# Optimization experiments

Measured on AMD Instinct MI355X. Metric: run time of the kernel, lower is better.

## Reference

```python
import jax, jax.numpy as jnp
import numpy as np


def setup_inputs() -> dict:
    key = jax.random.key(0)
    kx, kt = jax.random.split(key)
    b, n, d = 4, 4096, 1024
    x = jax.random.normal(kx, (b, n, d), dtype=jnp.float32)
    t = jax.random.normal(kt, (n, d), dtype=jnp.float32)
    return {"x": x, "t": t}


def reference(x, t):
    # y[b,i,d] = sum_{j<=i} t[i-j,d] * x[b,j,d]
    # Causal depthwise Toeplitz matvec == linear convolution truncated to n.
    # Computed via FFT along the sequence axis (zero-pad to 2n so the
    # circular convolution equals the linear one on the first n outputs).
    b, n, d = x.shape
    L = 2 * n
    xf = jnp.fft.rfft(x.astype(jnp.float32), n=L, axis=1)        # (b, L/2+1, d) complex
    tf = jnp.fft.rfft(t.astype(jnp.float32), n=L, axis=0)        # (L/2+1, d) complex
    y = jnp.fft.irfft(xf * tf[None], n=L, axis=1)[:, :n, :]      # (b, n, d)
    return y.astype(x.dtype)
```

## Files before the change

kernel.cpp:

```cpp
#include <hip/hip_runtime.h>

#define NT 512
#define SCL (1.0f / 8192.0f)
#define PI_F 3.14159265358979323846f

__device__ __forceinline__ int P(int i) { return i ^ ((i >> 5) & 31); }

__device__ __forceinline__ float2 cmul(float2 a, float2 b) {
  return make_float2(a.x * b.x - a.y * b.y, a.x * b.y + a.y * b.x);
}
__device__ __forceinline__ float2 csqr(float2 a) {
  return make_float2(a.x * a.x - a.y * a.y, 2.f * a.x * a.y);
}
__device__ __forceinline__ float2 cadd(float2 a, float2 b) { return make_float2(a.x + b.x, a.y + b.y); }
__device__ __forceinline__ float2 csub(float2 a, float2 b) { return make_float2(a.x - b.x, a.y - b.y); }
__device__ __forceinline__ float2 cmuli (float2 a) { return make_float2(-a.y,  a.x); }
__device__ __forceinline__ float2 cmulmi(float2 a) { return make_float2( a.y, -a.x); }

constexpr float RT2 = 0.70710678118654752440f;
constexpr float CQ1 = 0.92387953251128675613f;
constexpr float SQ1 = 0.38268343236508977173f;
constexpr float C8x[4] = {1.f,  RT2, 0.f, -RT2};
constexpr float C8y[4] = {0.f, -RT2, -1.f, -RT2};
constexpr float C16x[8] = {1.f,  CQ1,  RT2,  SQ1, 0.f, -SQ1, -RT2, -CQ1};
constexpr float C16y[8] = {0.f, -SQ1, -RT2, -CQ1, -1.f, -CQ1, -RT2, -SQ1};

template<bool UNIT>
__device__ __forceinline__ void r8_fwd(float2* e, float2 b) {
  float2 b2, b4;
  if (!UNIT) { b2 = csqr(b); b4 = csqr(b2); }
  #pragma unroll
  for (int j = 0; j < 4; ++j) {
    float2 u = e[j], v = e[j + 4];
    float2 d = csub(u, v);
    e[j] = cadd(u, v);
    float2 c8 = make_float2(C8x[j], C8y[j]);
    if (UNIT) e[j + 4] = (j == 0) ? d : cmul(d, c8);
    else      e[j + 4] = cmul(d, (j == 0) ? b : cmul(b, c8));
  }
  #pragma unroll
  for (int o = 0; o < 8; o += 4) {
    #pragma unroll
    for (int j = 0; j < 2; ++j) {
      float2 u = e[o + j], v = e[o + j + 2];
      float2 d = csub(u, v);
      e[o + j] = cadd(u, v);
      if (UNIT) e[o + j + 2] = (j == 0) ? d : cmulmi(d);
      else      e[o + j + 2] = cmul(d, (j == 0) ? b2 : cmulmi(b2));
    }
  }
  #pragma unroll
  for (int o = 0; o < 8; o += 2) {
    float2 u = e[o], v = e[o + 1];
    float2 d = csub(u, v);
    e[o] = cadd(u, v);
    e[o + 1] = UNIT ? d : cmul(d, b4);
  }
}

template<bool UNIT>
__device__ __forceinline__ void r8_inv(float2* e, float2 g) {
  float2 g2, g4;
  if (!UNIT) { g2 = csqr(g); g4 = csqr(g2); }
  #pragma unroll
  for (int o = 0; o < 8; o += 2) {
    float2 t = UNIT ? e[o + 1] : cmul(e[o + 1], g4);
    float2 u = e[o];
    e[o] = cadd(u, t); e[o + 1] = csub(u, t);
  }
  #pragma unroll
  for (int o = 0; o < 8; o += 4) {
    #pragma unroll
    for (int j = 0; j < 2; ++j) {
      float2 v = e[o + j + 2];
      float2 t;
      if (UNIT) t = (j == 0) ? v : cmuli(v);
      else      t = cmul(v, (j == 0) ? g2 : cmuli(g2));
      float2 u = e[o + j];
      e[o + j] = cadd(u, t); e[o + j + 2] = csub(u, t);
    }
  }
  #pragma unroll
  for (int j = 0; j < 4; ++j) {
    float2 v = e[j + 4];
    float2 t;
    float2 c8c = make_float2(C8x[j], -C8y[j]);
    if (UNIT) t = (j == 0) ? v : cmul(v, c8c);
    else      t = cmul(v, (j == 0) ? g : cmul(g, c8c));
    float2 u = e[j];
    e[j] = cadd(u, t); e[j + 4] = csub(u, t);
  }
}

__device__ __forceinline__ void d8f(float4* cb, int base, int G, float2 b) {
  float2 lo[8], hi[8];
  #pragma unroll
  for (int j = 0; j < 8; ++j) {
    float4 q = cb[P(base + G * j)];
    lo[j] = make_float2(q.x, q.y);
    hi[j] = make_float2(q.z, q.w);
  }
  r8_fwd<false>(lo, b);
  r8_fwd<false>(hi, b);
  #pragma unroll
  for (int j = 0; j < 8; ++j)
    cb[P(base + G * j)] = make_float4(lo[j].x, lo[j].y, hi[j].x, hi[j].y);
}

__device__ __forceinline__ void d8i(float4* cb, int base, int G, float2 g) {
  float2 lo[8], hi[8];
  #pragma unroll
  for (int j = 0; j < 8; ++j) {
    float4 q = cb[P(base + G * j)];
    lo[j] = make_float2(q.x, q.y);
    hi[j] = make_float2(q.z, q.w);
  }
  r8_inv<false>(lo, g);
  r8_inv<false>(hi, g);
  #pragma unroll
  for (int j = 0; j < 8; ++j)
    cb[P(base + G * j)] = make_float4(lo[j].x, lo[j].y, hi[j].x, hi[j].y);
}

__global__ __launch_bounds__(NT)
void that8h(const float* __restrict__ tT, float4* __restrict__ ThG) {
  __shared__ float4 cb[4096];
  const int tid = threadIdx.x;
  const int d = blockIdx.x;

  const int baseB = ((tid >> 6) << 9) + (tid & 63);
  const int baseC = ((tid >> 3) << 6) + (tid & 7);

  float s0, c0; __sincosf(-PI_F * (float)tid / 2048.f, &s0, &c0);
  const float2 bA = make_float2(c0, s0);
  float s1, c1; __sincosf(-PI_F * (float)(tid & 63) / 256.f, &s1, &c1);
  const float2 bB = make_float2(c1, s1);
  float s2, c2; __sincosf(-PI_F * (float)(tid & 7) / 32.f, &s2, &c2);
  const float2 bC = make_float2(c2, s2);
  float sw, cw; __sincosf(-PI_F * (float)tid / 4096.f, &sw, &cw);
  const float2 whi = make_float2(cw, sw);

  const float* tp = tT + (size_t)d * 4096;
  {
    float tv[8];
    #pragma unroll
    for (int j = 0; j < 8; ++j) tv[j] = tp[tid + 512 * j];
    float2 lo[8], hi[8];
    #pragma unroll
    for (int j = 0; j < 8; ++j) {
      lo[j] = make_float2(tv[j], 0.f);
      float2 w = (j == 0) ? whi : cmul(whi, make_float2(C16x[j], C16y[j]));
      hi[j] = make_float2(tv[j] * w.x, tv[j] * w.y);
    }
    r8_fwd<false>(lo, bA);
    r8_fwd<false>(hi, bA);
    #pragma unroll
    for (int j = 0; j < 8; ++j)
      cb[P(tid + 512 * j)] = make_float4(lo[j].x, lo[j].y, hi[j].x, hi[j].y);
  }
  __syncthreads();
  d8f(cb, baseB, 64, bB);  __syncthreads();
  d8f(cb, baseC, 8, bC);   __syncthreads();
  {
    float2 lo[8], hi[8];
    #pragma unroll
    for (int j = 0; j < 8; ++j) {
      float4 q = cb[P(tid * 8 + j)];
      lo[j] = make_float2(q.x, q.y);
      hi[j] = make_float2(q.z, q.w);
    }
    r8_fwd<true>(lo, make_float2(1.f, 0.f));
    r8_fwd<true>(hi, make_float2(1.f, 0.f));
    float4* thg = ThG + (size_t)d * 4096;
    #pragma unroll
    for (int j = 0; j < 8; ++j)
      thg[tid + 512 * j] = make_float4(lo[j].x * SCL, lo[j].y * SCL,
                                       hi[j].x * SCL, hi[j].y * SCL);
  }
}

__global__ __launch_bounds__(NT)
void fftconv(float* __restrict__ xT, const float4* __restrict__ ThG) {
  __shared__ float4 cb[4096];
  const int tid = threadIdx.x;
  const int d = blockIdx.x;
  const int pass = blockIdx.y;

  const int baseB = ((tid >> 6) << 9) + (tid & 63);
  const int baseC = ((tid >> 3) << 6) + (tid & 7);
  const float2 ONE = make_float2(1.f, 0.f);

  float s0, c0; __sincosf(-PI_F * (float)tid / 2048.f, &s0, &c0);
  const float2 bA = make_float2(c0, s0);
  const float2 gA = make_float2(c0, -s0);
  float s1, c1; __sincosf(-PI_F * (float)(tid & 63) / 256.f, &s1, &c1);
  const float2 bB = make_float2(c1, s1);
  const float2 gB = make_float2(c1, -s1);
  float s2, c2; __sincosf(-PI_F * (float)(tid & 7) / 32.f, &s2, &c2);
  const float2 bC = make_float2(c2, s2);
  const float2 gC = make_float2(c2, -s2);
  float sw, cw; __sincosf(-PI_F * (float)tid / 4096.f, &sw, &cw);
  const float2 whi  = make_float2(cw, sw);
  const float2 whic = make_float2(cw, -sw);

  float* r0 = xT + ((size_t)(2 * pass)     * 1024 + d) * 4096;
  float* r1 = xT + ((size_t)(2 * pass + 1) * 1024 + d) * 4096;
  const float4* thg = ThG + (size_t)d * 4096;

  {
    float2 xv[8], m[8];
    #pragma unroll
    for (int j = 0; j < 8; ++j) {
      int n = tid + 512 * j;
      xv[j] = make_float2(r0[n], r1[n]);
    }
    #pragma unroll
    for (int j = 0; j < 8; ++j) {
      float2 w = (j == 0) ? whi : cmul(whi, make_float2(C16x[j], C16y[j]));
      m[j] = cmul(xv[j], w);
    }
    r8_fwd<false>(xv, bA);
    r8_fwd<false>(m, bA);
    #pragma unroll
    for (int j = 0; j < 8; ++j)
      cb[P(tid + 512 * j)] = make_float4(xv[j].x, xv[j].y, m[j].x, m[j].y);
  }
  __syncthreads();

  d8f(cb, baseB, 64, bB);
  __syncthreads();

  float4 thq[8];
  #pragma unroll
  for (int j = 0; j < 8; ++j) thq[j] = thg[tid + 512 * j];
  d8f(cb, baseC, 8, bC);
  __syncthreads();

  {
    float2 lo[8], hi[8];
    #pragma unroll
    for (int j = 0; j < 8; ++j) {
      float4 q = cb[P(tid * 8 + j)];
      lo[j] = make_float2(q.x, q.y);
      hi[j] = make_float2(q.z, q.w);
    }
    r8_fwd<true>(lo, ONE);
    r8_fwd<true>(hi, ONE);
    #pragma unroll
    for (int j = 0; j < 8; ++j) {
      lo[j] = cmul(lo[j], make_float2(thq[j].x, thq[j].y));
      hi[j] = cmul(hi[j], make_float2(thq[j].z, thq[j].w));
    }
    r8_inv<true>(lo, ONE);
    r8_inv<true>(hi, ONE);
    #pragma unroll
    for (int j = 0; j < 8; ++j)
      cb[P(tid * 8 + j)] = make_float4(lo[j].x, lo[j].y, hi[j].x, hi[j].y);
  }
  __syncthreads();

  d8i(cb, baseC, 8, gC);
  __syncthreads();

  d8i(cb, baseB, 64, gB);
  __syncthreads();

  {
    float2 u[8], v[8];
    #pragma unroll
    for (int j = 0; j < 8; ++j) {
      float4 q = cb[P(tid + 512 * j)];
      u[j] = make_float2(q.x, q.y);
      v[j] = make_float2(q.z, q.w);
    }
    r8_inv<false>(u, gA);
    r8_inv<false>(v, gA);
    #pragma unroll
    for (int k = 0; k < 8; ++k) {
      float2 wc = (k == 0) ? whic : cmul(whic, make_float2(C16x[k], -C16y[k]));
      float2 t = cmul(v[k], wc);
      int n = tid + 512 * k;
      r0[n] = u[k].x + t.x;
      r1[n] = u[k].y + t.y;
    }
  }
}

__global__ __launch_bounds__(256)
void transpose64(const float* __restrict__ src, float* __restrict__ dst, int R, int C) {
  __shared__ float tile[64][65];
  int t  = threadIdx.x;
  int c4 = t & 15;
  int r  = t >> 4;
  size_t slab = (size_t)blockIdx.z * (size_t)R * (size_t)C;
  const float* s = src + slab;
  float* dd = dst + slab;
  int col0 = blockIdx.x * 64, row0 = blockIdx.y * 64;
  #pragma unroll
  for (int k = 0; k < 4; ++k) {
    int rr = r + 16 * k;
    const float4 v = *(const float4*)(s + (size_t)(row0 + rr) * C + col0 + 4 * c4);
    tile[rr][4 * c4 + 0] = v.x;
    tile[rr][4 * c4 + 1] = v.y;
    tile[rr][4 * c4 + 2] = v.z;
    tile[rr][4 * c4 + 3] = v.w;
  }
  __syncthreads();
  #pragma unroll
  for (int k = 0; k < 4; ++k) {
    int cc = r + 16 * k;
    float4 w;
    w.x = tile[4 * c4 + 0][cc];
    w.y = tile[4 * c4 + 1][cc];
    w.z = tile[4 * c4 + 2][cc];
    w.w = tile[4 * c4 + 3][cc];
    *(float4*)(dd + (size_t)(col0 + cc) * R + row0 + 4 * c4) = w;
  }
}

extern "C" void kernel_launch(void* const* d_in, const int* in_sizes, int n_in,
                              void* d_out, int out_size, void* d_ws, size_t ws_size,
                              hipStream_t stream) {
  const float* x = (const float*)d_in[0];
  const float* t = (const float*)d_in[1];
  float* out = (float*)d_out;
  float* ws  = (float*)d_ws;
  float* xT  = ws;
  float* tT  = ws + (size_t)4 * 1024 * 4096;
  float4* ThG = (float4*)d_out;

  transpose64<<<dim3(16, 64, 4), 256, 0, stream>>>(x, xT, 4096, 1024);
  transpose64<<<dim3(16, 64, 1), 256, 0, stream>>>(t, tT, 4096, 1024);

  that8h<<<dim3(1024), NT, 0, stream>>>(tT, ThG);
  fftconv<<<dim3(1024, 2), NT, 0, stream>>>(xT, ThG);

  transpose64<<<dim3(64, 16, 4), 256, 0, stream>>>(xT, out, 1024, 4096);
}
```

Baseline: 147.9 us.

## Fuse filter FFT into convolution kernel and keep spectrum in registers

```diff
diff --git a/kernel.cpp b/kernel.cpp
--- a/kernel.cpp
+++ b/kernel.cpp
@@ -123,68 +123,10 @@
 }
 
 __global__ __launch_bounds__(NT)
-void that8h(const float* __restrict__ tT, float4* __restrict__ ThG) {
+void fftconv(float* __restrict__ xT, const float* __restrict__ tT) {
   __shared__ float4 cb[4096];
   const int tid = threadIdx.x;
   const int d = blockIdx.x;
-
-  const int baseB = ((tid >> 6) << 9) + (tid & 63);
-  const int baseC = ((tid >> 3) << 6) + (tid & 7);
-
-  float s0, c0; __sincosf(-PI_F * (float)tid / 2048.f, &s0, &c0);
-  const float2 bA = make_float2(c0, s0);
-  float s1, c1; __sincosf(-PI_F * (float)(tid & 63) / 256.f, &s1, &c1);
-  const float2 bB = make_float2(c1, s1);
-  float s2, c2; __sincosf(-PI_F * (float)(tid & 7) / 32.f, &s2, &c2);
-  const float2 bC = make_float2(c2, s2);
-  float sw, cw; __sincosf(-PI_F * (float)tid / 4096.f, &sw, &cw);
-  const float2 whi = make_float2(cw, sw);
-
-  const float* tp = tT + (size_t)d * 4096;
-  {
-    float tv[8];
-    #pragma unroll
-    for (int j = 0; j < 8; ++j) tv[j] = tp[tid + 512 * j];
-    float2 lo[8], hi[8];
-    #pragma unroll
-    for (int j = 0; j < 8; ++j) {
-      lo[j] = make_float2(tv[j], 0.f);
-      float2 w = (j == 0) ? whi : cmul(whi, make_float2(C16x[j], C16y[j]));
-      hi[j] = make_float2(tv[j] * w.x, tv[j] * w.y);
-    }
-    r8_fwd<false>(lo, bA);
-    r8_fwd<false>(hi, bA);
-    #pragma unroll
-    for (int j = 0; j < 8; ++j)
-      cb[P(tid + 512 * j)] = make_float4(lo[j].x, lo[j].y, hi[j].x, hi[j].y);
-  }
-  __syncthreads();
-  d8f(cb, baseB, 64, bB);  __syncthreads();
-  d8f(cb, baseC, 8, bC);   __syncthreads();
-  {
-    float2 lo[8], hi[8];
-    #pragma unroll
-    for (int j = 0; j < 8; ++j) {
-      float4 q = cb[P(tid * 8 + j)];
-      lo[j] = make_float2(q.x, q.y);
-      hi[j] = make_float2(q.z, q.w);
-    }
-    r8_fwd<true>(lo, make_float2(1.f, 0.f));
-    r8_fwd<true>(hi, make_float2(1.f, 0.f));
-    float4* thg = ThG + (size_t)d * 4096;
-    #pragma unroll
-    for (int j = 0; j < 8; ++j)
-      thg[tid + 512 * j] = make_float4(lo[j].x * SCL, lo[j].y * SCL,
-                                       hi[j].x * SCL, hi[j].y * SCL);
-  }
-}
-
-__global__ __launch_bounds__(NT)
-void fftconv(float* __restrict__ xT, const float4* __restrict__ ThG) {
-  __shared__ float4 cb[4096];
-  const int tid = threadIdx.x;
-  const int d = blockIdx.x;
-  const int pass = blockIdx.y;
 
   const int baseB = ((tid >> 6) << 9) + (tid & 63);
   const int baseC = ((tid >> 3) << 6) + (tid & 7);
@@ -203,39 +145,28 @@
   const float2 whi  = make_float2(cw, sw);
   const float2 whic = make_float2(cw, -sw);
 
-  float* r0 = xT + ((size_t)(2 * pass)     * 1024 + d) * 4096;
-  float* r1 = xT + ((size_t)(2 * pass + 1) * 1024 + d) * 4096;
-  const float4* thg = ThG + (size_t)d * 4096;
-
+  float2 thL[8], thH[8];
   {
-    float2 xv[8], m[8];
+    const float* tp = tT + (size_t)d * 4096;
+    float tv[8];
+    #pragma unroll
+    for (int j = 0; j < 8; ++j) tv[j] = tp[tid + 512 * j];
+    float2 lo[8], hi[8];
     #pragma unroll
     for (int j = 0; j < 8; ++j) {
-      int n = tid + 512 * j;
-      xv[j] = make_float2(r0[n], r1[n]);
-    }
-    #pragma unroll
-    for (int j = 0; j < 8; ++j) {
+      lo[j] = make_float2(tv[j], 0.f);
       float2 w = (j == 0) ? whi : cmul(whi, make_float2(C16x[j], C16y[j]));
-      m[j] = cmul(xv[j], w);
-    }
-    r8_fwd<false>(xv, bA);
-    r8_fwd<false>(m, bA);
+      hi[j] = make_float2(tv[j] * w.x, tv[j] * w.y);
+    }
+    r8_fwd<false>(lo, bA);
+    r8_fwd<false>(hi, bA);
     #pragma unroll
     for (int j = 0; j < 8; ++j)
-      cb[P(tid + 512 * j)] = make_float4(xv[j].x, xv[j].y, m[j].x, m[j].y);
+      cb[P(tid + 512 * j)] = make_float4(lo[j].x, lo[j].y, hi[j].x, hi[j].y);
   }
   __syncthreads();
-
-  d8f(cb, baseB, 64, bB);
-  __syncthreads();
-
-  float4 thq[8];
-  #pragma unroll
-  for (int j = 0; j < 8; ++j) thq[j] = thg[tid + 512 * j];
-  d8f(cb, baseC, 8, bC);
-  __syncthreads();
-
+  d8f(cb, baseB, 64, bB);  __syncthreads();
+  d8f(cb, baseC, 8, bC);   __syncthreads();
   {
     float2 lo[8], hi[8];
     #pragma unroll
@@ -248,41 +179,92 @@
     r8_fwd<true>(hi, ONE);
     #pragma unroll
     for (int j = 0; j < 8; ++j) {
-      lo[j] = cmul(lo[j], make_float2(thq[j].x, thq[j].y));
-      hi[j] = cmul(hi[j], make_float2(thq[j].z, thq[j].w));
-    }
-    r8_inv<true>(lo, ONE);
-    r8_inv<true>(hi, ONE);
-    #pragma unroll
-    for (int j = 0; j < 8; ++j)
-      cb[P(tid * 8 + j)] = make_float4(lo[j].x, lo[j].y, hi[j].x, hi[j].y);
+      thL[j] = make_float2(lo[j].x * SCL, lo[j].y * SCL);
+      thH[j] = make_float2(hi[j].x * SCL, hi[j].y * SCL);
+    }
   }
   __syncthreads();
 
-  d8i(cb, baseC, 8, gC);
-  __syncthreads();
-
-  d8i(cb, baseB, 64, gB);
-  __syncthreads();
-
-  {
-    float2 u[8], v[8];
-    #pragma unroll
-    for (int j = 0; j < 8; ++j) {
-      float4 q = cb[P(tid + 512 * j)];
-      u[j] = make_float2(q.x, q.y);
-      v[j] = make_float2(q.z, q.w);
-    }
-    r8_inv<false>(u, gA);
-    r8_inv<false>(v, gA);
-    #pragma unroll
-    for (int k = 0; k < 8; ++k) {
-      float2 wc = (k == 0) ? whic : cmul(whic, make_float2(C16x[k], -C16y[k]));
-      float2 t = cmul(v[k], wc);
-      int n = tid + 512 * k;
-      r0[n] = u[k].x + t.x;
-      r1[n] = u[k].y + t.y;
-    }
+  #pragma unroll 1
+  for (int pass = 0; pass < 2; ++pass) {
+    float* r0 = xT + ((size_t)(2 * pass)     * 1024 + d) * 4096;
+    float* r1 = xT + ((size_t)(2 * pass + 1) * 1024 + d) * 4096;
+
+    {
+      float2 xv[8], m[8];
+      #pragma unroll
+      for (int j = 0; j < 8; ++j) {
+        int n = tid + 512 * j;
+        xv[j] = make_float2(r0[n], r1[n]);
+      }
+      #pragma unroll
+      for (int j = 0; j < 8; ++j) {
+        float2 w = (j == 0) ? whi : cmul(whi, make_float2(C16x[j], C16y[j]));
+        m[j] = cmul(xv[j], w);
+      }
+      r8_fwd<false>(xv, bA);
+      r8_fwd<false>(m, bA);
+      #pragma unroll
+      for (int j = 0; j < 8; ++j)
+        cb[P(tid + 512 * j)] = make_float4(xv[j].x, xv[j].y, m[j].x, m[j].y);
+    }
+    __syncthreads();
+
+    d8f(cb, baseB, 64, bB);
+    __syncthreads();
+
+    d8f(cb, baseC, 8, bC);
+    __syncthreads();
+
+    {
+      float2 lo[8], hi[8];
+      #pragma unroll
+      for (int j = 0; j < 8; ++j) {
+        float4 q = cb[P(tid * 8 + j)];
+        lo[j] = make_float2(q.x, q.y);
+        hi[j] = make_float2(q.z, q.w);
+      }
+      r8_fwd<true>(lo, ONE);
+      r8_fwd<true>(hi, ONE);
+      #pragma unroll
+      for (int j = 0; j < 8; ++j) {
+        lo[j] = cmul(lo[j], thL[j]);
+        hi[j] = cmul(hi[j], thH[j]);
+      }
+      r8_inv<true>(lo, ONE);
+      r8_inv<true>(hi, ONE);
+      #pragma unroll
+      for (int j = 0; j < 8; ++j)
+        cb[P(tid * 8 + j)] = make_float4(lo[j].x, lo[j].y, hi[j].x, hi[j].y);
+    }
+    __syncthreads();
+
+    d8i(cb, baseC, 8, gC);
+    __syncthreads();
+
+    d8i(cb, baseB, 64, gB);
+    __syncthreads();
+
+    {
+      float2 u[8], v[8];
+      #pragma unroll
+      for (int j = 0; j < 8; ++j) {
+        float4 q = cb[P(tid + 512 * j)];
+        u[j] = make_float2(q.x, q.y);
+        v[j] = make_float2(q.z, q.w);
+      }
+      r8_inv<false>(u, gA);
+      r8_inv<false>(v, gA);
+      #pragma unroll
+      for (int k = 0; k < 8; ++k) {
+        float2 wc = (k == 0) ? whic : cmul(whic, make_float2(C16x[k], -C16y[k]));
+        float2 t = cmul(v[k], wc);
+        int n = tid + 512 * k;
+        r0[n] = u[k].x + t.x;
+        r1[n] = u[k].y + t.y;
+      }
+    }
+    __syncthreads();
   }
 }
 
@@ -327,13 +309,11 @@
   float* ws  = (float*)d_ws;
   float* xT  = ws;
   float* tT  = ws + (size_t)4 * 1024 * 4096;
-  float4* ThG = (float4*)d_out;
 
   transpose64<<<dim3(16, 64, 4), 256, 0, stream>>>(x, xT, 4096, 1024);
   transpose64<<<dim3(16, 64, 1), 256, 0, stream>>>(t, tT, 4096, 1024);
 
-  that8h<<<dim3(1024), NT, 0, stream>>>(tT, ThG);
-  fftconv<<<dim3(1024, 2), NT, 0, stream>>>(xT, ThG);
+  fftconv<<<dim3(1024), NT, 0, stream>>>(xT, tT);
 
   transpose64<<<dim3(64, 16, 4), 256, 0, stream>>>(xT, out, 1024, 4096);
 }
```

Result: slower. 248.9 us (+68.3%).
